# Kernel tuning notes

Hardware: AMD Instinct MI355X
Metric: run time of the kernel (lower is better)

The kernel has to match this reference:

```python
import jax, jax.numpy as jnp
import numpy as np

N, H, T, L, D_IN, D_QK, D_V = 8, 8, 1024, 1024, 128, 128, 128


def setup_inputs() -> dict:
    key = jax.random.key(0)
    ks = jax.random.split(key, 12)
    s = 1.0 / np.sqrt(D_IN)
    sq = 1.0 / np.sqrt(D_QK)
    return {
        "X": jax.random.normal(ks[0], (N, H, L, D_IN), jnp.float32),
        "t1": jax.random.normal(ks[1], (N, T), jnp.float32),
        "Q": jax.random.normal(ks[2], (N, H, T, D_QK), jnp.float32),
        "Wk1": jax.random.normal(ks[3], (D_IN, D_QK), jnp.float32) * s,
        "bk1": jnp.zeros((D_QK,), jnp.float32),
        "Wk2": jax.random.normal(ks[4], (D_QK, D_QK), jnp.float32) * sq,
        "bk2": jnp.zeros((D_QK,), jnp.float32),
        "Wv1": jax.random.normal(ks[5], (D_IN, D_QK), jnp.float32) * s,
        "bv1": jnp.zeros((D_QK,), jnp.float32),
        "Wv2": jax.random.normal(ks[6], (D_QK, D_V), jnp.float32) * sq,
        "bv2": jnp.zeros((D_V,), jnp.float32),
        "log_tau": jnp.asarray(0.0, jnp.float32),  # log(init_tau=1)
    }


def _mlp(x, W1, b1, W2, b2):
    # MLP(d_in, [d_qk], d_out): Linear -> relu -> Linear
    return jax.nn.relu(x @ W1 + b1) @ W2 + b2


def reference(X, t1, Q, Wk1, bk1, Wk2, bk2, Wv1, bv1, Wv2, bv2, log_tau):
    t2 = X[:, 0, :, -1]                      # (N, L)
    K = _mlp(X, Wk1, bk1, Wk2, bk2)          # (N, H, L, d_qk)
    V = _mlp(X, Wv1, bv1, Wv2, bv2)          # (N, H, L, d_v)
    tau = jnp.exp(log_tau)
    # gaussian weight: -(Q.K)^2 / tau
    A = jnp.einsum('nhtc,nhlc->nhtl', Q, K)
    A = -(A * A) / tau
    mask = (t1[:, :, None] >= t2[:, None, :])[:, None, :, :]  # (N,1,T,L)
    A = jax.nn.softmax(A * mask, axis=-1) * mask
    return jnp.einsum('nhtl,nhlc->nhtc', A, V)
```

## Files before the change

### kernel.cpp

```cpp
#include <hip/hip_runtime.h>
#include <hip/hip_bf16.h>

typedef __bf16 bf16_t;
typedef _Float16 f16_t;
typedef bf16_t bf16x8 __attribute__((ext_vector_type(8)));
typedef f16_t  f16x8  __attribute__((ext_vector_type(8)));
typedef f16_t  f16x4  __attribute__((ext_vector_type(4)));
typedef float  floatx4 __attribute__((ext_vector_type(4)));
typedef float  floatx16 __attribute__((ext_vector_type(16)));
typedef bf16x8 bf16x8u __attribute__((aligned(8)));
typedef f16x8  f16x8u  __attribute__((aligned(8)));

#define DEV static __device__ __forceinline__

DEV floatx4 mfma16_bf16(bf16x8 a, bf16x8 b, floatx4 c) {
  return __builtin_amdgcn_mfma_f32_16x16x32_bf16(a, b, c, 0, 0, 0);
}
DEV floatx4 mfma16_f16(f16x8 a, f16x8 b, floatx4 c) {
  return __builtin_amdgcn_mfma_f32_16x16x32_f16(a, b, c, 0, 0, 0);
}
DEV floatx4 mfma16x16_f16(f16x4 a, f16x4 b, floatx4 c) {
  return __builtin_amdgcn_mfma_f32_16x16x16f16(a, b, c, 0, 0, 0);
}
DEV void async_ld16(void* lds, const void* g) {
  __builtin_amdgcn_global_load_lds(
      (const __attribute__((address_space(1))) unsigned int*)g,
      (__attribute__((address_space(3))) unsigned int*)lds, 16, 0, 0);
}
DEV float fast_exp2(float x) {
  float r;
  asm("v_exp_f32 %0, %1" : "=v"(r) : "v"(x));
  return r;
}

__global__ void prep_kernel(const float* __restrict__ Wk1, const float* __restrict__ Wk2,
                            const float* __restrict__ Wv1, const float* __restrict__ Wv2,
                            const float* __restrict__ X,
                            bf16_t* __restrict__ W1p, bf16_t* __restrict__ W2p,
                            f16_t* __restrict__ W3f, f16_t* __restrict__ W4f,
                            float* __restrict__ t2pre) {
  int b = blockIdx.x;
  if (b < 16) {
    int m = b >> 2, p = b & 3;
    const float* src = m == 0 ? Wk1 : m == 1 ? Wk2 : m == 2 ? Wv1 : Wv2;
    __shared__ float tile[32][129];
    for (int u = 0; u < 4; ++u) {
      int idx = threadIdx.x + u * 256;
      int k = idx >> 5, n4 = (idx & 31) << 2;
      float4 v = *(const float4*)(src + (size_t)(p * 32 + k) * 128 + n4);
      tile[k][n4 + 0] = v.x; tile[k][n4 + 1] = v.y;
      tile[k][n4 + 2] = v.z; tile[k][n4 + 3] = v.w;
    }
    __syncthreads();
    if (m < 2) {
      bf16_t* dst = m ? W2p : W1p;
      for (int u = 0; u < 2; ++u) {
        int idx = threadIdx.x + u * 256;
        int n = idx >> 2, kc = idx & 3;
        bf16x8 hi, lo;
        for (int j = 0; j < 8; ++j) {
          float v = tile[kc * 8 + j][n];
          bf16_t hh = (bf16_t)v;
          hi[j] = hh;
          lo[j] = (bf16_t)(v - (float)hh);
        }
        *(bf16x8*)(dst + n * 128 + p * 32 + kc * 8) = hi;
        *(bf16x8*)(dst + 16384 + n * 128 + p * 32 + kc * 8) = lo;
      }
    } else {
      f16_t* dst = (m == 3) ? W4f : W3f;
      for (int u = 0; u < 2; ++u) {
        int idx = threadIdx.x + u * 256;
        int n = idx >> 2, kc = idx & 3;
        f16x8 w;
        for (int j = 0; j < 8; ++j) w[j] = (f16_t)tile[kc * 8 + j][n];
        *(f16x8*)(dst + n * 128 + p * 32 + kc * 8) = w;
      }
    }
  } else {
    int i = (b - 16) * 256 + threadIdx.x;
    t2pre[i] = X[((size_t)(i >> 10) * 8192 + (i & 1023)) * 128 + 127];
  }
}

__global__ __launch_bounds__(256) void mlp_k_kernel(
    const float* __restrict__ X, const float* __restrict__ b1,
    const float* __restrict__ b2, const bf16_t* __restrict__ W1p,
    const bf16_t* __restrict__ W2p, bf16_t* __restrict__ Khi,
    bf16_t* __restrict__ Klo) {
  __shared__ __align__(16) char sXbuf[2 * 16896];
  __shared__ __align__(16) bf16_t sW[2][256 * 40];
  bf16_t* sXh = (bf16_t*)sXbuf;
  bf16_t* sXl = sXh + 64 * 132;

  const int tid = threadIdx.x, lane = tid & 63, wave = tid >> 6;
  const int q = lane >> 4, c15 = lane & 15;
  const size_t rowBase = (size_t)blockIdx.x * 64;

  int goff[5];
  for (int a = 0; a < 5; ++a) {
    int o = (wave + 4 * a) * 1024 + lane * 16;
    int row = o / 80, rem = o % 80;
    goff[a] = row * 256 + (rem < 64 ? rem : 0);
  }
  auto issueW = [&](int buf, int ph) {
    const bf16_t* Wp = (ph < 4) ? W1p : W2p;
    const char* base = (const char*)Wp + (ph & 3) * 64;
    for (int a = 0; a < 5; ++a)
      async_ld16((char*)sW[buf] + (wave + 4 * a) * 1024 + lane * 16, base + goff[a]);
  };

  issueW(0, 0);

  float b1v[8], b2v[8];
  for (int nt = 0; nt < 8; ++nt) { b1v[nt] = b1[nt * 16 + c15]; b2v[nt] = b2[nt * 16 + c15]; }

  for (int u = 0; u < 8; ++u) {
    int idx = tid + u * 256;
    int r = idx >> 5, c4 = (idx & 31) << 2;
    float4 v = *(const float4*)(X + (rowBase + r) * 128 + c4);
    int o = r * 132 + c4;
    float vv[4] = {v.x, v.y, v.z, v.w};
    for (int i = 0; i < 4; ++i) {
      bf16_t h = (bf16_t)vv[i];
      sXh[o + i] = h;
      sXl[o + i] = (bf16_t)(vv[i] - (float)h);
    }
  }

  floatx4 acc1[8], acc2[8];
  for (int i = 0; i < 8; ++i) { acc1[i] = {}; acc2[i] = {}; }

  __syncthreads();
#pragma unroll
  for (int ph = 0; ph < 8; ++ph) {
    if (ph < 7) issueW((ph + 1) & 1, ph + 1);
    const bf16_t* wb = sW[ph & 1];
    const int kq = ph & 3;
    floatx4* acc = (ph < 4) ? acc1 : acc2;
    const int ao = (wave * 16 + c15) * 132 + kq * 32 + q * 8;
    bf16x8 ah = *(const bf16x8u*)(sXh + ao);
    bf16x8 al = *(const bf16x8u*)(sXl + ao);
    for (int nt = 0; nt < 8; ++nt) {
      const int bo = (nt * 16 + c15) * 40 + q * 8;
      bf16x8 bh = *(const bf16x8*)(wb + bo);
      bf16x8 bl = *(const bf16x8*)(wb + 128 * 40 + bo);
      acc[nt] = mfma16_bf16(ah, bh, acc[nt]);
      acc[nt] = mfma16_bf16(ah, bl, acc[nt]);
      acc[nt] = mfma16_bf16(al, bh, acc[nt]);
    }
    if (ph == 3) {
      for (int nt = 0; nt < 8; ++nt)
        for (int r = 0; r < 4; ++r) {
          float h = fmaxf(acc1[nt][r] + b1v[nt], 0.f);
          bf16_t hh = (bf16_t)h;
          int o = (wave * 16 + q * 4 + r) * 132 + nt * 16 + c15;
          sXh[o] = hh;
          sXl[o] = (bf16_t)(h - (float)hh);
        }
    }
    __syncthreads();
  }

  for (int nt = 0; nt < 8; ++nt)
    for (int r = 0; r < 4; ++r) {
      float kv = acc2[nt][r] + b2v[nt];
      bf16_t kh = (bf16_t)kv;
      int o = (wave * 16 + q * 4 + r) * 132 + nt * 16 + c15;
      sXh[o] = kh;
      sXl[o] = (bf16_t)(kv - (float)kh);
    }
  __syncthreads();
  for (int u = 0; u < 4; ++u) {
    int idx = tid + u * 256;
    int r = idx >> 4, c8 = (idx & 15) << 3;
    bf16x8 vh = *(const bf16x8u*)(sXh + r * 132 + c8);
    bf16x8 vl = *(const bf16x8u*)(sXl + r * 132 + c8);
    *(bf16x8*)(Khi + (rowBase + r) * 128 + c8) = vh;
    *(bf16x8*)(Klo + (rowBase + r) * 128 + c8) = vl;
  }
}

__global__ __launch_bounds__(256) void mlp_v_kernel(
    const float* __restrict__ X, const float* __restrict__ b1,
    const float* __restrict__ b2, const f16_t* __restrict__ W1f,
    const f16_t* __restrict__ W2f, f16_t* __restrict__ Vt) {
  __shared__ __align__(16) f16_t sXf[64 * 136];
  __shared__ __align__(16) f16_t sW[2][128 * 40];

  const int tid = threadIdx.x, lane = tid & 63, wave = tid >> 6;
  const int q = lane >> 4, c15 = lane & 15;
  const size_t rowBase = (size_t)blockIdx.x * 64;

  int goff[3];
  for (int a = 0; a < 3; ++a) {
    int o = (wave + 4 * a) * 1024 + lane * 16;
    int row = o / 80, rem = o % 80;
    goff[a] = row * 256 + (rem < 64 ? rem : 0);
  }
  auto issueV = [&](int buf, int ph) {
    const f16_t* Wp = (ph < 4) ? W1f : W2f;
    const char* base = (const char*)Wp + (ph & 3) * 64;
    for (int a = 0; a < 3; ++a) {
      int j = wave + 4 * a;
      if (j < 10) async_ld16((char*)sW[buf] + j * 1024 + lane * 16, base + goff[a]);
    }
  };

  issueV(0, 0);

  float b1v[8], bvv[2][4];
  for (int nt = 0; nt < 8; ++nt) b1v[nt] = b1[nt * 16 + c15];
  for (int mt = 0; mt < 2; ++mt)
    for (int r = 0; r < 4; ++r)
      bvv[mt][r] = b2[(wave * 2 + mt) * 16 + q * 4 + r];

  for (int u = 0; u < 8; ++u) {
    int idx = tid + u * 256;
    int r = idx >> 5, c4 = (idx & 31) << 2;
    float4 v = *(const float4*)(X + (rowBase + r) * 128 + c4);
    int o = r * 136 + c4;
    sXf[o + 0] = (f16_t)v.x; sXf[o + 1] = (f16_t)v.y;
    sXf[o + 2] = (f16_t)v.z; sXf[o + 3] = (f16_t)v.w;
  }

  floatx4 acc1[8], acc2[2][4];
  for (int i = 0; i < 8; ++i) acc1[i] = {};
  for (int i = 0; i < 2; ++i) for (int j = 0; j < 4; ++j) acc2[i][j] = {};

  __syncthreads();
#pragma unroll
  for (int ph = 0; ph < 8; ++ph) {
    if (ph < 7) issueV((ph + 1) & 1, ph + 1);
    const f16_t* wb = sW[ph & 1];
    const int kq = ph & 3;
    if (ph < 4) {
      f16x8 a = *(const f16x8u*)(sXf + (wave * 16 + c15) * 136 + kq * 32 + q * 8);
      for (int nt = 0; nt < 8; ++nt) {
        f16x8 bb = *(const f16x8*)(wb + (nt * 16 + c15) * 40 + q * 8);
        acc1[nt] = mfma16_f16(a, bb, acc1[nt]);
      }
      if (ph == 3) {
        for (int nt = 0; nt < 8; ++nt)
          for (int r = 0; r < 4; ++r)
            sXf[(wave * 16 + q * 4 + r) * 136 + nt * 16 + c15] =
                (f16_t)fmaxf(acc1[nt][r] + b1v[nt], 0.f);
      }
    } else {
      f16x8 aw0 = *(const f16x8*)(wb + ((wave * 2 + 0) * 16 + c15) * 40 + q * 8);
      f16x8 aw1 = *(const f16x8*)(wb + ((wave * 2 + 1) * 16 + c15) * 40 + q * 8);
      for (int nt = 0; nt < 4; ++nt) {
        f16x8 bh = *(const f16x8u*)(sXf + (nt * 16 + c15) * 136 + kq * 32 + q * 8);
        acc2[0][nt] = mfma16_f16(aw0, bh, acc2[0][nt]);
        acc2[1][nt] = mfma16_f16(aw1, bh, acc2[1][nt]);
      }
    }
    __syncthreads();
  }

  f16_t* sVT = sXf;
  for (int mt = 0; mt < 2; ++mt)
    for (int nt = 0; nt < 4; ++nt)
      for (int r = 0; r < 4; ++r) {
        int c = (wave * 2 + mt) * 16 + q * 4 + r;
        sVT[c * 68 + nt * 16 + c15] = (f16_t)(acc2[mt][nt][r] + bvv[mt][r]);
      }
  __syncthreads();
  const int nh = (int)(rowBase >> 10);
  const int lB = (int)(rowBase & 1023);
  for (int u = 0; u < 4; ++u) {
    int idx = tid + u * 256;
    int c = idx >> 3, l8 = (idx & 7) << 3;
    *(f16x8*)(Vt + ((size_t)nh * 128 + c) * 1024 + lB + l8) =
        *(const f16x8u*)(sVT + c * 68 + l8);
  }
}

__global__ __launch_bounds__(512, 4) void attn_kernel(
    const float* __restrict__ Q, const float* __restrict__ t1,
    const float* __restrict__ t2pre, const float* __restrict__ ltau,
    const bf16_t* __restrict__ Khi, const bf16_t* __restrict__ Klo,
    const f16_t* __restrict__ Vt, float* __restrict__ out) {
  __shared__ __align__(16) char sBuf[3][24576];
  __shared__ __align__(16) float sT2[1024];

  const int tid = threadIdx.x, lane = tid & 63, wave = tid >> 6;
  const int q = lane >> 4, r15 = lane & 15;
  const int nh = blockIdx.x & 63;
  const int seg = blockIdx.x >> 6;
  const int n = nh >> 3;
  const int qbase = seg * 128 + wave * 16;
  const float negc2 = -__expf(-ltau[0]) * 1.44269504f;

  const char* gp[3]; int ls[3]; int st[3];
  for (int a = 0; a < 3; ++a) {
    int j = wave + 8 * a;
    if (j < 16) {
      int o = j * 1024 + lane * 16;
      int half = o >> 13;
      int r2 = o & 8191;
      int row = r2 >> 8;
      int s = (r2 >> 4) & 15;
      int g = s ^ (row & 15);
      gp[a] = (const char*)(half ? Klo : Khi) +
              ((size_t)((nh << 10) + row)) * 256 + (g << 4);
      st[a] = 8192; ls[a] = o;
    } else {
      int o = (j - 16) * 1024 + lane * 16;
      int d = o >> 6;
      int u = (o >> 4) & 3;
      int up = u ^ (d & 3);
      gp[a] = (const char*)Vt + ((size_t)((nh << 7) + d)) * 2048 + (up << 4);
      st[a] = 64; ls[a] = 16384 + o;
    }
  }
  auto stage = [&](int buf) {
    for (int a = 0; a < 3; ++a) { async_ld16(sBuf[buf] + ls[a], gp[a]); gp[a] += st[a]; }
  };

  float2 t2v2 = *(const float2*)(t2pre + (n << 10) + tid * 2);
  const float t1v = t1[(n << 10) + qbase + r15];
  bf16x8 qh[4], ql[4];
  {
    const float* qr = Q + ((size_t)(nh << 10) + qbase + r15) * 128;
    for (int kq = 0; kq < 4; ++kq) {
      const float* p = qr + kq * 32 + q * 8;
      float4 v0 = *(const float4*)p;
      float4 v1 = *(const float4*)(p + 4);
      float vv[8] = {v0.x, v0.y, v0.z, v0.w, v1.x, v1.y, v1.z, v1.w};
      bf16x8 hi, lo;
      for (int j = 0; j < 8; ++j) {
        bf16_t hj = (bf16_t)vv[j];
        hi[j] = hj;
        lo[j] = (bf16_t)(vv[j] - (float)hj);
      }
      qh[kq] = hi;
      ql[kq] = lo;
    }
  }
  stage(0);
  stage(1);
  *(float2*)(sT2 + tid * 2) = t2v2;

  floatx4 O[8];
  for (int i = 0; i < 8; ++i) O[i] = {};
  float ds = 0.f;

  asm volatile("s_waitcnt vmcnt(3) lgkmcnt(0)" ::: "memory");
  __builtin_amdgcn_s_barrier();
  asm volatile("" ::: "memory");

  for (int it = 0; it < 32; ++it) {
    if (it <= 29) stage((it + 2) % 3);
    const char* kb = sBuf[it % 3];
    const char* vb = kb + 16384;

    floatx4 Sa = {}, Sb = {};
    __builtin_amdgcn_s_setprio(1);
#pragma unroll
    for (int kq = 0; kq < 4; ++kq) {
      const int un = (((kq << 2) + q) ^ r15) << 4;
      const int boA = r15 * 256 + un;
      const int boB = (16 + r15) * 256 + un;
      bf16x8 kha = *(const bf16x8*)(kb + boA);
      bf16x8 kla = *(const bf16x8*)(kb + 8192 + boA);
      bf16x8 khb = *(const bf16x8*)(kb + boB);
      bf16x8 klb = *(const bf16x8*)(kb + 8192 + boB);
      Sa = mfma16_bf16(kha, qh[kq], Sa);
      Sa = mfma16_bf16(kla, qh[kq], Sa);
      Sa = mfma16_bf16(kha, ql[kq], Sa);
      Sb = mfma16_bf16(khb, qh[kq], Sb);
      Sb = mfma16_bf16(klb, qh[kq], Sb);
      Sb = mfma16_bf16(khb, ql[kq], Sb);
    }
    __builtin_amdgcn_s_setprio(0);

    const float* t2b = sT2 + it * 32 + 4 * q;
#pragma unroll
    for (int c1 = 0; c1 < 2; ++c1) {
      floatx4 Sv = c1 ? Sb : Sa;
      float4 tv4 = *(const float4*)(t2b + c1 * 16);
      float tv[4] = {tv4.x, tv4.y, tv4.z, tv4.w};
      f16x4 pb;
      for (int j = 0; j < 4; ++j) {
        float s = Sv[j];
        float e = fast_exp2(s * s * negc2);
        bool m = (t1v >= tv[j]);
        ds += m ? e : 1.f;
        pb[j] = (f16_t)(m ? e : 0.f);
      }
      const int v = q + (c1 << 2);
      const int vo = (((v >> 1) ^ (r15 & 3)) << 4) + ((v & 1) << 3);
#pragma unroll
      for (int dt = 0; dt < 8; ++dt) {
        f16x4 va = *(const f16x4*)(vb + (dt * 16 + r15) * 64 + vo);
        O[dt] = mfma16x16_f16(va, pb, O[dt]);
      }
    }

    if (it <= 29) {
      asm volatile("s_waitcnt vmcnt(3)" ::: "memory");
    } else if (it == 30) {
      asm volatile("s_waitcnt vmcnt(0)" ::: "memory");
    }
    if (it < 31) {
      asm volatile("" ::: "memory");
      __builtin_amdgcn_s_barrier();
      asm volatile("" ::: "memory");
    }
  }

  ds += __shfl_xor(ds, 16);
  ds += __shfl_xor(ds, 32);
  const float inv = 1.f / ds;
  float* orow = out + ((size_t)(nh << 10) + qbase + r15) * 128;
#pragma unroll
  for (int dt = 0; dt < 8; ++dt) {
    float4 v = {O[dt][0] * inv, O[dt][1] * inv, O[dt][2] * inv, O[dt][3] * inv};
    *(float4*)(orow + dt * 16 + 4 * q) = v;
  }
}

extern "C" void kernel_launch(void* const* d_in, const int* in_sizes, int n_in,
                              void* d_out, int out_size, void* d_ws, size_t ws_size,
                              hipStream_t stream) {
  const float* X   = (const float*)d_in[0];
  const float* t1  = (const float*)d_in[1];
  const float* Q   = (const float*)d_in[2];
  const float* Wk1 = (const float*)d_in[3];
  const float* bk1 = (const float*)d_in[4];
  const float* Wk2 = (const float*)d_in[5];
  const float* bk2 = (const float*)d_in[6];
  const float* Wv1 = (const float*)d_in[7];
  const float* bv1 = (const float*)d_in[8];
  const float* Wv2 = (const float*)d_in[9];
  const float* bv2 = (const float*)d_in[10];
  const float* log_tau = (const float*)d_in[11];
  float* out = (float*)d_out;

  const size_t E = (size_t)64 * 1024 * 128;
  bf16_t* Khi = (bf16_t*)d_ws;
  bf16_t* Klo = Khi + E;
  f16_t*  Vt  = (f16_t*)(Klo + E);
  bf16_t* W1p = (bf16_t*)((char*)d_ws + 3 * E * 2);
  bf16_t* W2p = W1p + 32768;
  f16_t*  W3f = (f16_t*)(W2p + 32768);
  f16_t*  W4f = W3f + 16384;
  float*  t2pre = (float*)(W4f + 16384);

  prep_kernel<<<48, 256, 0, stream>>>(Wk1, Wk2, Wv1, Wv2, X, W1p, W2p, W3f, W4f, t2pre);
  mlp_k_kernel<<<1024, 256, 0, stream>>>(X, bk1, bk2, W1p, W2p, Khi, Klo);
  mlp_v_kernel<<<1024, 256, 0, stream>>>(X, bv1, bv2, W3f, W4f, Vt);
  attn_kernel<<<512, 512, 0, stream>>>(Q, t1, t2pre, log_tau, Khi, Klo, Vt, out);
}
```

Before: 247.4 us.

## Store V in MFMA-fragment order and load it directly to registers

The V MLP kernel now writes V in a fragment-major layout matching the MFMA A-operand per lane, instead of a transposed row layout. The attention kernel drops V from the LDS staging ring, shrinking LDS buffers, and each wave loads its 16 V fragments straight from global memory into registers at the start of every iteration. This removes LDS traffic and shared-memory space for V, but every wave now redundantly fetches the same V tile from global or L2 memory and relies on the loads completing before the MFMAs that use them, which adds register pressure.

```diff
diff --git a/kernel.cpp b/kernel.cpp
--- a/kernel.cpp
+++ b/kernel.cpp
@@ -184,7 +184,7 @@
 __global__ __launch_bounds__(256) void mlp_v_kernel(
     const float* __restrict__ X, const float* __restrict__ b1,
     const float* __restrict__ b2, const f16_t* __restrict__ W1f,
-    const f16_t* __restrict__ W2f, f16_t* __restrict__ Vt) {
+    const f16_t* __restrict__ W2f, f16_t* __restrict__ Vf) {
   __shared__ __align__(16) f16_t sXf[64 * 136];
   __shared__ __align__(16) f16_t sW[2][128 * 40];
 
@@ -266,13 +266,18 @@
         sVT[c * 68 + nt * 16 + c15] = (f16_t)(acc2[mt][nt][r] + bvv[mt][r]);
       }
   __syncthreads();
-  const int nh = (int)(rowBase >> 10);
-  const int lB = (int)(rowBase & 1023);
-  for (int u = 0; u < 4; ++u) {
-    int idx = tid + u * 256;
-    int c = idx >> 3, l8 = (idx & 7) << 3;
-    *(f16x8*)(Vt + ((size_t)nh * 128 + c) * 1024 + lB + l8) =
-        *(const f16x8u*)(sVT + c * 68 + l8);
+  const int nhV = (int)(rowBase >> 10);
+  const int itB = (int)((rowBase & 1023) >> 5);
+  char* vfB = (char*)Vf + (((size_t)nhV * 32 + itB) << 13);
+  for (int u = 0; u < 8; ++u) {
+    int idx = u * 256 + tid;
+    int itl = idx >> 10;
+    int f   = (idx >> 6) & 15;
+    int l   = idx & 63;
+    int d   = (f & 7) * 16 + (l & 15);
+    int Ll  = itl * 32 + (f >> 3) * 16 + ((l >> 4) << 2);
+    f16x4 v = *(const f16x4*)(sVT + d * 68 + Ll);
+    *(f16x4*)(vfB + (size_t)((((itl << 4) + f) << 9) + (l << 3))) = v;
   }
 }
 
@@ -280,8 +285,8 @@
     const float* __restrict__ Q, const float* __restrict__ t1,
     const float* __restrict__ t2pre, const float* __restrict__ ltau,
     const bf16_t* __restrict__ Khi, const bf16_t* __restrict__ Klo,
-    const f16_t* __restrict__ Vt, float* __restrict__ out) {
-  __shared__ __align__(16) char sBuf[3][24576];
+    const f16_t* __restrict__ Vf, float* __restrict__ out) {
+  __shared__ __align__(16) char sBuf[3][16384];
   __shared__ __align__(16) float sT2[1024];
 
   const int tid = threadIdx.x, lane = tid & 63, wave = tid >> 6;
@@ -292,30 +297,21 @@
   const int qbase = seg * 128 + wave * 16;
   const float negc2 = -__expf(-ltau[0]) * 1.44269504f;
 
-  const char* gp[3]; int ls[3]; int st[3];
-  for (int a = 0; a < 3; ++a) {
+  const char* gp[2]; int ls[2];
+  for (int a = 0; a < 2; ++a) {
     int j = wave + 8 * a;
-    if (j < 16) {
-      int o = j * 1024 + lane * 16;
-      int half = o >> 13;
-      int r2 = o & 8191;
-      int row = r2 >> 8;
-      int s = (r2 >> 4) & 15;
-      int g = s ^ (row & 15);
-      gp[a] = (const char*)(half ? Klo : Khi) +
-              ((size_t)((nh << 10) + row)) * 256 + (g << 4);
-      st[a] = 8192; ls[a] = o;
-    } else {
-      int o = (j - 16) * 1024 + lane * 16;
-      int d = o >> 6;
-      int u = (o >> 4) & 3;
-      int up = u ^ (d & 3);
-      gp[a] = (const char*)Vt + ((size_t)((nh << 7) + d)) * 2048 + (up << 4);
-      st[a] = 64; ls[a] = 16384 + o;
-    }
+    int o = j * 1024 + lane * 16;
+    int half = o >> 13;
+    int r2 = o & 8191;
+    int row = r2 >> 8;
+    int s = (r2 >> 4) & 15;
+    int g = s ^ (row & 15);
+    gp[a] = (const char*)(half ? Klo : Khi) +
+            ((size_t)((nh << 10) + row)) * 256 + (g << 4);
+    ls[a] = o;
   }
   auto stage = [&](int buf) {
-    for (int a = 0; a < 3; ++a) { async_ld16(sBuf[buf] + ls[a], gp[a]); gp[a] += st[a]; }
+    for (int a = 0; a < 2; ++a) { async_ld16(sBuf[buf] + ls[a], gp[a]); gp[a] += 8192; }
   };
 
   float2 t2v2 = *(const float2*)(t2pre + (n << 10) + tid * 2);
@@ -342,18 +338,23 @@
   stage(1);
   *(float2*)(sT2 + tid * 2) = t2v2;
 
+  const char* vfb = (const char*)Vf + ((size_t)nh << 18) + lane * 8;
+
   floatx4 O[8];
   for (int i = 0; i < 8; ++i) O[i] = {};
   float ds = 0.f;
 
-  asm volatile("s_waitcnt vmcnt(3) lgkmcnt(0)" ::: "memory");
+  asm volatile("s_waitcnt vmcnt(2) lgkmcnt(0)" ::: "memory");
   __builtin_amdgcn_s_barrier();
   asm volatile("" ::: "memory");
 
   for (int it = 0; it < 32; ++it) {
+    const char* vtb = vfb + ((size_t)it << 13);
+    f16x4 vr[16];
+#pragma unroll
+    for (int f = 0; f < 16; ++f) vr[f] = *(const f16x4*)(vtb + (f << 9));
     if (it <= 29) stage((it + 2) % 3);
     const char* kb = sBuf[it % 3];
-    const char* vb = kb + 16384;
 
     floatx4 Sa = {}, Sb = {};
     __builtin_amdgcn_s_setprio(1);
@@ -389,20 +390,11 @@
         ds += m ? e : 1.f;
         pb[j] = (f16_t)(m ? e : 0.f);
       }
-      const int v = q + (c1 << 2);
-      const int vo = (((v >> 1) ^ (r15 & 3)) << 4) + ((v & 1) << 3);
-#pragma unroll
-      for (int dt = 0; dt < 8; ++dt) {
-        f16x4 va = *(const f16x4*)(vb + (dt * 16 + r15) * 64 + vo);
-        O[dt] = mfma16x16_f16(va, pb, O[dt]);
-      }
-    }
-
-    if (it <= 29) {
-      asm volatile("s_waitcnt vmcnt(3)" ::: "memory");
-    } else if (it == 30) {
-      asm volatile("s_waitcnt vmcnt(0)" ::: "memory");
-    }
+#pragma unroll
+      for (int dt = 0; dt < 8; ++dt)
+        O[dt] = mfma16x16_f16(vr[c1 * 8 + dt], pb, O[dt]);
+    }
+
     if (it < 31) {
       asm volatile("" ::: "memory");
       __builtin_amdgcn_s_barrier();
@@ -441,7 +433,7 @@
   const size_t E = (size_t)64 * 1024 * 128;
   bf16_t* Khi = (bf16_t*)d_ws;
   bf16_t* Klo = Khi + E;
-  f16_t*  Vt  = (f16_t*)(Klo + E);
+  f16_t*  Vf  = (f16_t*)(Klo + E);
   bf16_t* W1p = (bf16_t*)((char*)d_ws + 3 * E * 2);
   bf16_t* W2p = W1p + 32768;
   f16_t*  W3f = (f16_t*)(W2p + 32768);
@@ -450,6 +442,6 @@
 
   prep_kernel<<<48, 256, 0, stream>>>(Wk1, Wk2, Wv1, Wv2, X, W1p, W2p, W3f, W4f, t2pre);
   mlp_k_kernel<<<1024, 256, 0, stream>>>(X, bk1, bk2, W1p, W2p, Khi, Klo);
-  mlp_v_kernel<<<1024, 256, 0, stream>>>(X, bv1, bv2, W3f, W4f, Vt);
-  attn_kernel<<<512, 512, 0, stream>>>(Q, t1, t2pre, log_tau, Khi, Klo, Vt, out);
-}
+  mlp_v_kernel<<<1024, 256, 0, stream>>>(X, bv1, bv2, W3f, W4f, Vf);
+  attn_kernel<<<512, 512, 0, stream>>>(Q, t1, t2pre, log_tau, Khi, Klo, Vf, out);
+}
```

Result: slower. 288.7 us (+16.7%).
